# Optimization experiments

Hardware: AMD Instinct MI355X
Metric: run time of the kernel (lower is better)

Reference implementation:

```python
import jax, jax.numpy as jnp
import numpy as np

SIGMA = 0.1
SIG2 = SIGMA * SIGMA  # sigma^2


def _gauss_conv(x, y, b):
    # x: BxNxD, y: BxKxD, b: BxKxd -> BxNxd
    # K_ij = exp(-||x_i - y_j||^2 / (2 sigma^2)); out_i = sum_j K_ij b_j
    d2 = jnp.sum((x[:, :, None, :] - y[:, None, :, :]) ** 2, axis=-1)  # BxNxK
    K = jnp.exp(-d2 / (2.0 * SIG2))
    return jnp.einsum('bnk,bkd->bnd', K, b)


def _gauss_grad(p, x):
    # grad-of-kernel N-body sum (py=px=p, y=x as in grad_kernel(mom, pos)):
    # out_i = sum_j <p_i, p_j> * grad_{x_i} K(x_i, x_j)
    #       = sum_j <p_i, p_j> * K_ij * (-(x_i - x_j) / sigma^2)
    diff = x[:, :, None, :] - x[:, None, :, :]            # BxNxKxD
    d2 = jnp.sum(diff ** 2, axis=-1)                      # BxNxK
    K = jnp.exp(-d2 / (2.0 * SIG2))
    C = jnp.einsum('bnd,bkd->bnk', p, p)                  # <p_i, p_j>
    return jnp.einsum('bnk,bnkd->bnd', -(K * C) / SIG2, diff)


def setup_inputs() -> dict:
    key = jax.random.key(0)
    k1, k2 = jax.random.split(key)
    B, N, D = 1, 8192, 3
    mom = jax.random.normal(k1, (B, N, D), dtype=jnp.float32)
    pos = jax.random.normal(k2, (B, N, D), dtype=jnp.float32)
    return {"mom": mom, "pos": pos}


def reference(mom, pos):
    # variational_evolve: (dmom/dt, dpos/dt) = (-grad_kernel(mom,pos), kernel(pos,pos,mom))
    dmom = -_gauss_grad(mom, pos)
    dpos = _gauss_conv(pos, pos, mom)
    return (dmom, dpos)
```

## Files before the change

### kernel.cpp

```cpp
#include <hip/hip_runtime.h>


#define NPTS  8192
#define NCXY  16
#define NCZ   32
#define NCELL (NCXY * NCXY * NCZ)
#define ORIGIN    (-4.0f)
#define EDGE      0.5f
#define INV_EDGE  2.0f
#define INV_EDGEZ 4.0f
#define RCUT2     0.25f

#define A_DOT 144.269504088896f
#define INV_ADOT (1.0f / 144.269504088896f)
#define A_R   (-72.134752044448f)
#define INV_SIG2 100.0f

#define EXP2(x) __builtin_amdgcn_exp2f(x)

__device__ __forceinline__ int clampi(int c, int hi) { return min(max(c, 0), hi); }

__device__ __forceinline__ int cell_of(float x, float y, float z) {
    const int cx = clampi((int)floorf((x - ORIGIN) * INV_EDGE),  NCXY - 1);
    const int cy = clampi((int)floorf((y - ORIGIN) * INV_EDGE),  NCXY - 1);
    const int cz = clampi((int)floorf((z - ORIGIN) * INV_EDGEZ), NCZ  - 1);
    return (cx * NCXY + cy) * NCZ + cz;
}

template <int CTRL, int ROW, int BANK>
__device__ __forceinline__ float dpp_add(float x) {
    const int r = __builtin_amdgcn_update_dpp(0, __float_as_int(x),
                                              CTRL, ROW, BANK, false);
    return x + __int_as_float(r);
}
__device__ __forceinline__ float wave64_sum(float x) {
    x = dpp_add<0x111, 0xf, 0xf>(x);
    x = dpp_add<0x112, 0xf, 0xf>(x);
    x = dpp_add<0x114, 0xf, 0xe>(x);
    x = dpp_add<0x118, 0xf, 0xc>(x);
    x = dpp_add<0x142, 0xa, 0xf>(x);
    x = dpp_add<0x143, 0xc, 0xf>(x);
    return x;
}

__global__ __launch_bounds__(1024)
void k_countscan(const float* __restrict__ pos,
                 int* __restrict__ start, int* __restrict__ cur)
{
    __shared__ int cnt[NCELL];
    __shared__ int wtot[16];
    __shared__ int wexcl[16];
    const int t = threadIdx.x;
    const int lane = t & 63;
    const int wid = t >> 6;

    #pragma unroll
    for (int k = 0; k < NCELL / 1024; ++k) cnt[t + k * 1024] = 0;
    __syncthreads();

    {
        const float4* pv = reinterpret_cast<const float4*>(pos) + 6 * t;
        float4 v0 = pv[0], v1 = pv[1], v2 = pv[2];
        float4 v3 = pv[3], v4 = pv[4], v5 = pv[5];
        const float px[8] = {v0.x, v0.w, v1.z, v2.y, v3.x, v3.w, v4.z, v5.y};
        const float py[8] = {v0.y, v1.x, v1.w, v2.z, v3.y, v4.x, v4.w, v5.z};
        const float pz[8] = {v0.z, v1.y, v2.x, v2.w, v3.z, v4.y, v5.x, v5.w};
        #pragma unroll
        for (int k = 0; k < 8; ++k)
            atomicAdd(&cnt[cell_of(px[k], py[k], pz[k])], 1);
    }
    __syncthreads();

    int pre[8];
    int s = 0;
    #pragma unroll
    for (int k = 0; k < 8; ++k) { pre[k] = s; s += cnt[8*t + k]; }
    int p = s;
    #pragma unroll
    for (int off = 1; off < 64; off <<= 1) {
        const int v = __shfl_up(p, off);
        if (lane >= off) p += v;
    }
    if (lane == 63) wtot[wid] = p;
    __syncthreads();
    if (t < 16) {
        const int w = wtot[t];
        int q = w;
        #pragma unroll
        for (int off = 1; off < 16; off <<= 1) {
            const int v = __shfl_up(q, off);
            if (t >= off) q += v;
        }
        wexcl[t] = q - w;
    }
    __syncthreads();
    const int base = wexcl[wid] + (p - s);
    #pragma unroll
    for (int k = 0; k < 8; ++k) {
        const int v = base + pre[k];
        start[8*t + k] = v;
        cur[8*t + k] = v;
    }
    if (t == 0) start[NCELL] = NPTS;
}

__global__ __launch_bounds__(256)
void k_scatter(const float* __restrict__ mom, const float* __restrict__ pos,
               int* __restrict__ cur,
               float* __restrict__ pmP, float* __restrict__ pmM,
               int* __restrict__ inv)
{
    const int i = blockIdx.x * 256 + threadIdx.x;
    const float x = pos[3*i+0], y = pos[3*i+1], z = pos[3*i+2];
    const int dst = atomicAdd(&cur[cell_of(x, y, z)], 1);
    const float r2 = x*x + y*y + z*z;
    reinterpret_cast<float4*>(pmP)[dst] = make_float4(A_DOT*x, A_DOT*y, A_DOT*z, A_R*r2);
    reinterpret_cast<float4*>(pmM)[dst] = make_float4(mom[3*i+0], mom[3*i+1], mom[3*i+2], 0.0f);
    inv[dst] = i;
}

__global__ __launch_bounds__(64)
void k_main(const float* __restrict__ pmP, const float* __restrict__ pmM,
            const int* __restrict__ inv, const int* __restrict__ start,
            float* __restrict__ out)
{
    const int wid  = blockIdx.x;
    const int lane = threadIdx.x;

    const float4* __restrict__ pmPv = reinterpret_cast<const float4*>(pmP);
    const float4* __restrict__ pmMv = reinterpret_cast<const float4*>(pmM);

    const float4 Pi = pmPv[wid];
    const float4 Mi = pmMv[wid];
    const float xi = Pi.x * INV_ADOT, yi = Pi.y * INV_ADOT, zi = Pi.z * INV_ADOT;
    const float pxi = Mi.x, pyi = Mi.y, pzi = Mi.z;
    const float ci  = Pi.w;

    const int cx = clampi((int)floorf((xi - ORIGIN) * INV_EDGE), NCXY - 1);
    const int cy = clampi((int)floorf((yi - ORIGIN) * INV_EDGE), NCXY - 1);

    int st_l = 0, len_l = 0;
    if (lane < 9) {
        const int nx = cx + (lane / 3) - 1;
        const int ny = cy + (lane % 3) - 1;
        if (nx >= 0 && nx < NCXY && ny >= 0 && ny < NCXY) {
            const float X0 = ORIGIN + nx * EDGE;
            const float Y0 = ORIGIN + ny * EDGE;
            const float dx = fmaxf(fmaxf(X0 - xi, xi - (X0 + EDGE)), 0.0f);
            const float dy = fmaxf(fmaxf(Y0 - yi, yi - (Y0 + EDGE)), 0.0f);
            const float m2 = dx * dx + dy * dy;
            if (m2 <= RCUT2) {
                const float zr = __builtin_sqrtf(RCUT2 - m2);
                const int z0 = clampi((int)floorf((zi - zr - ORIGIN) * INV_EDGEZ), NCZ - 1);
                const int z1 = clampi((int)floorf((zi + zr - ORIGIN) * INV_EDGEZ), NCZ - 1);
                const int base = (nx * NCXY + ny) * NCZ;
                st_l  = start[base + z0];
                len_l = start[base + z1 + 1] - st_l;
            }
        }
    }

    int p0[9], ofs[9];
    int run = 0;
    #pragma unroll
    for (int q = 0; q < 9; ++q) {
        const int ln = __builtin_amdgcn_readlane(len_l, q);
        const int st = __builtin_amdgcn_readlane(st_l, q);
        p0[q]  = run;
        ofs[q] = st - run;
        run   += ln;
    }
    const int T = run;

    float S = 0.f, SPx = 0.f, SPy = 0.f, SPz = 0.f;
    float apx = 0.f, apy = 0.f, apz = 0.f;

    for (int f0 = 0; f0 < T; f0 += 64) {
        const int f = f0 + lane;
        int off_sel = ofs[0];
        #pragma unroll
        for (int q = 1; q < 9; ++q)
            off_sel = (f >= p0[q]) ? ofs[q] : off_sel;
        if (f < T) {
            const int j = f + off_sel;
            const float4 P = pmPv[j];
            const float4 M = pmMv[j];
            float arg = __builtin_fmaf(zi, P.z, ci + P.w);
            arg = __builtin_fmaf(yi, P.y, arg);
            arg = __builtin_fmaf(xi, P.x, arg);
            const float K = EXP2(arg);
            const float C = __builtin_fmaf(pzi, M.z,
                              __builtin_fmaf(pyi, M.y, pxi * M.x));
            const float s = K * C;
            S += s;
            SPx = __builtin_fmaf(s, P.x, SPx);
            SPy = __builtin_fmaf(s, P.y, SPy);
            SPz = __builtin_fmaf(s, P.z, SPz);
            apx = __builtin_fmaf(K, M.x, apx);
            apy = __builtin_fmaf(K, M.y, apy);
            apz = __builtin_fmaf(K, M.z, apz);
        }
    }

    S   = wave64_sum(S);
    SPx = wave64_sum(SPx);
    SPy = wave64_sum(SPy);
    SPz = wave64_sum(SPz);
    apx = wave64_sum(apx);
    apy = wave64_sum(apy);
    apz = wave64_sum(apz);

    if (lane == 63) {
        const int oi = inv[wid];
        const float us = INV_SIG2 / A_DOT;
        out[3*oi+0] = INV_SIG2 * xi * S - us * SPx;
        out[3*oi+1] = INV_SIG2 * yi * S - us * SPy;
        out[3*oi+2] = INV_SIG2 * zi * S - us * SPz;
        out[3*NPTS + 3*oi+0] = apx;
        out[3*NPTS + 3*oi+1] = apy;
        out[3*NPTS + 3*oi+2] = apz;
    }
}

extern "C" void kernel_launch(void* const* d_in, const int* in_sizes, int n_in,
                              void* d_out, int out_size, void* d_ws, size_t ws_size,
                              hipStream_t stream)
{
    const float* mom = (const float*)d_in[0];
    const float* pos = (const float*)d_in[1];
    float* out = (float*)d_out;

    float* pmP  = (float*)d_ws;
    float* pmM  = pmP + (size_t)4 * NPTS;
    int* inv    = (int*)(pmM + (size_t)4 * NPTS);
    int* start  = inv + NPTS;
    int* cur    = start + NCELL + 1;

    k_countscan<<<1, 1024, 0, stream>>>(pos, start, cur);
    k_scatter<<<NPTS / 256, 256, 0, stream>>>(mom, pos, cur, pmP, pmM, inv);
    k_main<<<NPTS, 64, 0, stream>>>(pmP, pmM, inv, start, out);
}
```

Before: 23.40 us.

## Split cell histogram across blocks and software-prefetch neighbor loads

The single-block count-and-scan kernel becomes two kernels. Eight blocks each build a partial histogram of the cell counts, and a separate one-block kernel reduces those partials and scans them. In the main kernel, the neighbor float4 loads for the next 64-wide chunk are issued before the current chunk is computed, which overlaps memory latency with the exp and FMA work. The cost is one extra kernel launch, an 8x larger partial-count array to read, and out-of-range prefetch indices that are clamped to stay within bounds.

```diff
diff --git a/kernel.cpp b/kernel.cpp
--- a/kernel.cpp
+++ b/kernel.cpp
@@ -5,6 +5,7 @@
 #define NCXY  16
 #define NCZ   32
 #define NCELL (NCXY * NCXY * NCZ)
+#define NHB   8
 #define ORIGIN    (-4.0f)
 #define EDGE      0.5f
 #define INV_EDGE  2.0f
@@ -44,37 +45,50 @@
 }
 
 __global__ __launch_bounds__(1024)
-void k_countscan(const float* __restrict__ pos,
-                 int* __restrict__ start, int* __restrict__ cur)
+void k_hist8(const float* __restrict__ pos, int* __restrict__ partial)
 {
     __shared__ int cnt[NCELL];
+    const int b = blockIdx.x;
+    const int t = threadIdx.x;
+
+    #pragma unroll
+    for (int k = 0; k < NCELL / 1024; ++k) cnt[t + k * 1024] = 0;
+    __syncthreads();
+
+    const int i = b * 1024 + t;
+    atomicAdd(&cnt[cell_of(pos[3*i+0], pos[3*i+1], pos[3*i+2])], 1);
+    __syncthreads();
+
+    #pragma unroll
+    for (int k = 0; k < NCELL / 1024; ++k) {
+        const int c = t + k * 1024;
+        partial[c * NHB + b] = cnt[c];
+    }
+}
+
+__global__ __launch_bounds__(1024)
+void k_scan(const int* __restrict__ partial,
+            int* __restrict__ start, int* __restrict__ cur)
+{
     __shared__ int wtot[16];
     __shared__ int wexcl[16];
     const int t = threadIdx.x;
     const int lane = t & 63;
     const int wid = t >> 6;
 
-    #pragma unroll
-    for (int k = 0; k < NCELL / 1024; ++k) cnt[t + k * 1024] = 0;
-    __syncthreads();
-
-    {
-        const float4* pv = reinterpret_cast<const float4*>(pos) + 6 * t;
-        float4 v0 = pv[0], v1 = pv[1], v2 = pv[2];
-        float4 v3 = pv[3], v4 = pv[4], v5 = pv[5];
-        const float px[8] = {v0.x, v0.w, v1.z, v2.y, v3.x, v3.w, v4.z, v5.y};
-        const float py[8] = {v0.y, v1.x, v1.w, v2.z, v3.y, v4.x, v4.w, v5.z};
-        const float pz[8] = {v0.z, v1.y, v2.x, v2.w, v3.z, v4.y, v5.x, v5.w};
-        #pragma unroll
-        for (int k = 0; k < 8; ++k)
-            atomicAdd(&cnt[cell_of(px[k], py[k], pz[k])], 1);
-    }
-    __syncthreads();
+    const int4* pp = reinterpret_cast<const int4*>(partial);
+    int cnt8[8];
+    #pragma unroll
+    for (int k = 0; k < 8; ++k) {
+        const int4 a = pp[16 * t + 2 * k + 0];
+        const int4 b = pp[16 * t + 2 * k + 1];
+        cnt8[k] = a.x + a.y + a.z + a.w + b.x + b.y + b.z + b.w;
+    }
 
     int pre[8];
     int s = 0;
     #pragma unroll
-    for (int k = 0; k < 8; ++k) { pre[k] = s; s += cnt[8*t + k]; }
+    for (int k = 0; k < 8; ++k) { pre[k] = s; s += cnt8[k]; }
     int p = s;
     #pragma unroll
     for (int off = 1; off < 64; off <<= 1) {
@@ -175,16 +189,24 @@
     float S = 0.f, SPx = 0.f, SPy = 0.f, SPz = 0.f;
     float apx = 0.f, apy = 0.f, apz = 0.f;
 
+    int f = lane;
+    int osel = ofs[0];
+    #pragma unroll
+    for (int q = 1; q < 9; ++q) osel = (f >= p0[q]) ? ofs[q] : osel;
+    int j = min(f + osel, NPTS - 1);
+    float4 P = pmPv[j];
+    float4 M = pmMv[j];
+
     for (int f0 = 0; f0 < T; f0 += 64) {
-        const int f = f0 + lane;
-        int off_sel = ofs[0];
+        const int fn = f0 + 64 + lane;
+        int oseln = ofs[0];
         #pragma unroll
-        for (int q = 1; q < 9; ++q)
-            off_sel = (f >= p0[q]) ? ofs[q] : off_sel;
-        if (f < T) {
-            const int j = f + off_sel;
-            const float4 P = pmPv[j];
-            const float4 M = pmMv[j];
+        for (int q = 1; q < 9; ++q) oseln = (fn >= p0[q]) ? ofs[q] : oseln;
+        const int jn = min(fn + oseln, NPTS - 1);
+        const float4 Pn = pmPv[jn];
+        const float4 Mn = pmMv[jn];
+
+        if (f0 + lane < T) {
             float arg = __builtin_fmaf(zi, P.z, ci + P.w);
             arg = __builtin_fmaf(yi, P.y, arg);
             arg = __builtin_fmaf(xi, P.x, arg);
@@ -200,6 +222,7 @@
             apy = __builtin_fmaf(K, M.y, apy);
             apz = __builtin_fmaf(K, M.z, apz);
         }
+        P = Pn; M = Mn;
     }
 
     S   = wave64_sum(S);
@@ -230,13 +253,15 @@
     const float* pos = (const float*)d_in[1];
     float* out = (float*)d_out;
 
-    float* pmP  = (float*)d_ws;
-    float* pmM  = pmP + (size_t)4 * NPTS;
-    int* inv    = (int*)(pmM + (size_t)4 * NPTS);
-    int* start  = inv + NPTS;
-    int* cur    = start + NCELL + 1;
-
-    k_countscan<<<1, 1024, 0, stream>>>(pos, start, cur);
+    float* pmP   = (float*)d_ws;
+    float* pmM   = pmP + (size_t)4 * NPTS;
+    int* inv     = (int*)(pmM + (size_t)4 * NPTS);
+    int* start   = inv + NPTS;
+    int* cur     = start + NCELL + 1;
+    int* partial = cur + NCELL;
+
+    k_hist8<<<NHB, 1024, 0, stream>>>(pos, partial);
+    k_scan<<<1, 1024, 0, stream>>>(partial, start, cur);
     k_scatter<<<NPTS / 256, 256, 0, stream>>>(mom, pos, cur, pmP, pmM, inv);
     k_main<<<NPTS, 64, 0, stream>>>(pmP, pmM, inv, start, out);
 }
```

After: 35.21 us. 1.5x slower.
